# Kernel tuning notes

Measured on AMD Instinct MI355X. Metric: run time of the kernel, lower is better.

Reference implementation:

```python
import jax, jax.numpy as jnp
import numpy as np

N_ITEM, N_USER = 100000, 50000
D, H = 128, 8
DH = D // H
E1, E2 = 500000, 250000
NCNT = 51  # num_cnt_embeddings = cnt.max()+1
EPS = 1e-5


def setup_inputs() -> dict:
    key = jax.random.key(0)
    ks = jax.random.split(key, 32)
    r = lambda i, s: jax.random.normal(ks[i], s, dtype=jnp.float32)
    w = lambda i, s: jax.random.normal(ks[i], s, dtype=jnp.float32) * (1.0 / np.sqrt(s[-1]))
    return {
        # node features
        "ft_item": r(0, (N_ITEM, D)),
        "ft_user": r(1, (N_USER, D)),
        # hetero-level batch norm params (training-mode batch stats)
        "bn_g_item": jnp.ones((D,), jnp.float32), "bn_b_item": jnp.zeros((D,), jnp.float32),
        "bn_g_user": jnp.ones((D,), jnp.float32), "bn_b_user": jnp.zeros((D,), jnp.float32),
        # etype 'i2i' (item -> item), has cnt edge embedding
        "Wq1": w(2, (D, D)), "bq1": jnp.zeros((D,), jnp.float32),
        "Wk1": w(3, (D, D)), "Wv1": w(4, (D, D)),
        "ae1": r(5, (1, D)),
        "emb_cnt1": r(6, (NCNT, D)) * 0.1,
        # etype 'u2i' (user -> item), no cnt
        "Wq2": w(7, (D, D)), "bq2": jnp.zeros((D,), jnp.float32),
        "Wk2": w(8, (D, D)), "Wv2": w(9, (D, D)),
        "ae2": r(10, (1, D)),
        # vtype 'item' output transforms
        "W_agg": w(11, (D, D)), "b_agg": jnp.zeros((D,), jnp.float32),
        "W_self": w(12, (D, D)),
        # edges (eid order)
        "uid1": jax.random.randint(ks[13], (E1,), 0, N_ITEM, dtype=jnp.int32),
        "vid1": jax.random.randint(ks[14], (E1,), 0, N_ITEM, dtype=jnp.int32),
        "cnt1": jax.random.randint(ks[15], (E1,), 0, NCNT, dtype=jnp.int32),
        "uid2": jax.random.randint(ks[16], (E2,), 0, N_USER, dtype=jnp.int32),
        "vid2": jax.random.randint(ks[17], (E2,), 0, N_ITEM, dtype=jnp.int32),
    }


def _bn(x, g, b):
    mu = x.mean(0)
    var = x.var(0)
    return (x - mu) * jax.lax.rsqrt(var + EPS) * g + b


def _edge_scores(q_src, k_dst, uid, vid, attn_e, ft_e=None):
    # u_add_v gather, optional edge feature, gated per-head score [E, H]
    e = q_src[uid] + k_dst[vid]
    if ft_e is not None:
        e = e + ft_e
    e = attn_e * jax.nn.sigmoid(e)
    return e.reshape(-1, H, DH).sum(-1)


def reference(ft_item, ft_user, bn_g_item, bn_b_item, bn_g_user, bn_b_user,
              Wq1, bq1, Wk1, Wv1, ae1, emb_cnt1,
              Wq2, bq2, Wk2, Wv2, ae2,
              W_agg, b_agg, W_self,
              uid1, vid1, cnt1, uid2, vid2):
    xi = _bn(ft_item, bn_g_item, bn_b_item)   # item features (src and dst)
    xu = _bn(ft_user, bn_g_user, bn_b_user)   # user features (src only)

    # etype 'i2i': utype=item, vtype=item (ft_dst = xi, full graph)
    q1 = xi @ Wq1.T + bq1
    k1 = xi @ Wk1.T
    v1 = (xi @ Wv1.T).reshape(N_ITEM, H, DH)
    e1 = _edge_scores(q1, k1, uid1, vid1, ae1, ft_e=emb_cnt1[cnt1])  # [E1, H]

    # etype 'u2i': utype=user, vtype=item
    q2 = xu @ Wq2.T + bq2
    k2 = xi @ Wk2.T
    v2 = (xu @ Wv2.T).reshape(N_USER, H, DH)
    e2 = _edge_scores(q2, k2, uid2, vid2, ae2)  # [E2, H]

    # combined heterograph: offset user src ids by num item src nodes
    src = jnp.concatenate([uid1, uid2 + N_ITEM])
    dst = jnp.concatenate([vid1, vid2])
    val = jnp.concatenate([v1, v2], axis=0)        # [N_ITEM+N_USER, H, DH]
    sc = jnp.concatenate([e1, e2], axis=0)         # [E, H]

    # edge_softmax over incoming edges of each dst node (per head)
    m = jax.lax.stop_gradient(jax.ops.segment_max(sc, dst, num_segments=N_ITEM))
    ex = jnp.exp(sc - m[dst])
    s = jax.ops.segment_sum(ex, dst, num_segments=N_ITEM)
    a = ex / s[dst]                                # [E, H]

    # u_mul_e_sum: weighted scatter-sum of source values to dst
    agg = jax.ops.segment_sum(val[src] * a[:, :, None], dst,
                              num_segments=N_ITEM).reshape(N_ITEM, D)

    return jax.nn.relu(agg @ W_agg.T + b_agg + xi @ W_self.T)
```

## Files before the change

kernel.cpp:

```cpp
#include <hip/hip_runtime.h>
#include <hip/hip_bf16.h>

#define N_ITEM 100000
#define N_USER 50000
#define N_ALL  150000
#define E1N 500000
#define E2N 250000
#define EALL (E1N + E2N)
#define NPAD 100352

static constexpr size_t OFF_STATS = 0;
static constexpr size_t OFF_HIST  = 2048;
static constexpr size_t OFF_SCALE = OFF_HIST + (size_t)NPAD * 4;
static constexpr size_t OFF_M     = OFF_SCALE + 2048;
static constexpr size_t OFF_EMBB  = OFF_M + 64;
static constexpr size_t OFF_WPACK = OFF_EMBB + 13312;
static constexpr size_t OFF_QC    = OFF_WPACK + 8ull * 32768ull;
static constexpr size_t OFF_VC    = OFF_QC + (size_t)N_ALL * 256;
static constexpr size_t OFF_K1    = OFF_VC + (size_t)N_ALL * 256;
static constexpr size_t OFF_K2    = OFF_K1 + (size_t)N_ITEM * 256;
static constexpr size_t OFF_SELF  = OFF_K2 + (size_t)N_ITEM * 256;
static constexpr size_t OFF_START = OFF_SELF + (size_t)N_ITEM * 256;
static constexpr size_t OFF_CURSOR= OFF_START + (size_t)NPAD * 4;
static constexpr size_t OFF_BSUM  = OFF_CURSOR + (size_t)NPAD * 4;
static constexpr size_t OFF_ORD   = OFF_BSUM + 1024;
static constexpr size_t OFF_AGG   = OFF_ORD + (size_t)EALL * 8 + 128;

__device__ __forceinline__ float bf2f(unsigned short u) {
    return __uint_as_float(((unsigned)u) << 16);
}
__device__ __forceinline__ unsigned short f2bf(float f) {
    unsigned u = __float_as_uint(f);
    u += 0x7fffu + ((u >> 16) & 1u);
    return (unsigned short)(u >> 16);
}

typedef __attribute__((ext_vector_type(8))) short bf16x8;
typedef __attribute__((ext_vector_type(4))) float f32x4;

struct ProArgs {
    const float* w[8];
    const float* ft_item;
    const float* ft_user;
    const float* emb;
    const int* vid1;
    const int* vid2;
};
#define PRO_STAT 384
#define PRO_HIST 733
#define PRO_PACK 64
#define PRO_EMB  7

__global__ __launch_bounds__(256) void prologue(ProArgs A, char* __restrict__ ws) {
    __shared__ float r1[4][128], r2[4][128];
    int b = blockIdx.x, tid = threadIdx.x;
    if (b < PRO_STAT) {
        int type = (b >= 256) ? 1 : 0;
        int xb = type ? (b - 256) : b;
        int nb = type ? 128 : 256;
        const float* x = type ? A.ft_user : A.ft_item;
        int N = type ? N_USER : N_ITEM;
        float* sum = (float*)(ws + OFF_STATS) + type * 256;
        float* sq  = sum + 128;
        int c4 = (tid & 31) * 4;
        int rg = tid >> 5;
        int step = nb * 8;
        float s0 = 0.f, s1 = 0.f, s2 = 0.f, s3 = 0.f;
        float q0 = 0.f, q1 = 0.f, q2 = 0.f, q3 = 0.f;
        #pragma unroll 4
        for (int r = xb * 8 + rg; r < N; r += step) {
            float4 v = *(const float4*)(x + (size_t)r * 128 + c4);
            s0 += v.x; s1 += v.y; s2 += v.z; s3 += v.w;
            q0 = fmaf(v.x, v.x, q0); q1 = fmaf(v.y, v.y, q1);
            q2 = fmaf(v.z, v.z, q2); q3 = fmaf(v.w, v.w, q3);
        }
        s0 += __shfl_xor(s0, 32); s1 += __shfl_xor(s1, 32);
        s2 += __shfl_xor(s2, 32); s3 += __shfl_xor(s3, 32);
        q0 += __shfl_xor(q0, 32); q1 += __shfl_xor(q1, 32);
        q2 += __shfl_xor(q2, 32); q3 += __shfl_xor(q3, 32);
        int wv = tid >> 6;
        if ((tid & 63) < 32) {
            *(float4*)&r1[wv][c4] = make_float4(s0, s1, s2, s3);
            *(float4*)&r2[wv][c4] = make_float4(q0, q1, q2, q3);
        }
        __syncthreads();
        if (tid < 128) {
            float a  = r1[0][tid] + r1[1][tid] + r1[2][tid] + r1[3][tid];
            float bb = r2[0][tid] + r2[1][tid] + r2[2][tid] + r2[3][tid];
            atomicAdd(&sum[tid], a);
            atomicAdd(&sq[tid], bb);
        }
    } else if (b < PRO_STAT + PRO_HIST) {
        int e4 = ((b - PRO_STAT) * 256 + tid) * 4;
        if (e4 < EALL) {
            int* hist = (int*)(ws + OFF_HIST);
            int4 v;
            if (e4 < E1N) v = *(const int4*)(A.vid1 + e4);
            else          v = *(const int4*)(A.vid2 + (e4 - E1N));
            atomicAdd(&hist[v.x], 1);
            atomicAdd(&hist[v.y], 1);
            atomicAdd(&hist[v.z], 1);
            atomicAdd(&hist[v.w], 1);
        }
    } else if (b < PRO_STAT + PRO_HIST + PRO_PACK) {
        unsigned short* dst = (unsigned short*)(ws + OFF_WPACK);
        int gid = (b - PRO_STAT - PRO_HIST) * 256 + tid;
        int m = gid >> 11, rem = gid & 2047;
        int t = rem >> 8, kt = (rem >> 6) & 3, lane = rem & 63;
        int n = t * 16 + (lane & 15);
        int k0 = kt * 32 + (lane >> 4) * 8;
        const float* wrow = A.w[m] + n * 128 + k0;
        float4 w0 = *(const float4*)wrow;
        float4 w1 = *(const float4*)(wrow + 4);
        ushort4 o0 = make_ushort4(f2bf(w0.x), f2bf(w0.y), f2bf(w0.z), f2bf(w0.w));
        ushort4 o1 = make_ushort4(f2bf(w1.x), f2bf(w1.y), f2bf(w1.z), f2bf(w1.w));
        *(ushort4*)(dst + (size_t)gid * 8)     = o0;
        *(ushort4*)(dst + (size_t)gid * 8 + 4) = o1;
    } else {
        int gid = (b - PRO_STAT - PRO_HIST - PRO_PACK) * 256 + tid;
        if (gid * 4 < 51 * 128) {
            float4 v = *(const float4*)(A.emb + gid * 4);
            ushort4 o = make_ushort4(f2bf(v.x), f2bf(v.y), f2bf(v.z), f2bf(v.w));
            *(ushort4*)((unsigned short*)(ws + OFF_EMBB) + gid * 4) = o;
        }
    }
}

__global__ __launch_bounds__(1024) void scan_partial(char* __restrict__ ws) {
    __shared__ int sd[1024];
    const int* hist = (const int*)(ws + OFF_HIST);
    int* start  = (int*)(ws + OFF_START);
    int* cursor = (int*)(ws + OFF_CURSOR);
    int* bsum   = (int*)(ws + OFF_BSUM);
    int t = threadIdx.x;
    int gid = blockIdx.x * 1024 + t;
    int v = hist[gid];
    sd[t] = v;
    __syncthreads();
    #pragma unroll
    for (int off = 1; off < 1024; off <<= 1) {
        int x = (t >= off) ? sd[t - off] : 0;
        __syncthreads();
        sd[t] += x;
        __syncthreads();
    }
    int ex = sd[t] - v;
    start[gid] = ex;
    cursor[gid] = ex;
    if (t == 1023) bsum[blockIdx.x] = sd[t];
}

__global__ __launch_bounds__(256) void mid(const float* __restrict__ g_i, const float* __restrict__ b_i,
                                           const float* __restrict__ g_u, const float* __restrict__ b_u,
                                           const float* __restrict__ ae1, const float* __restrict__ ae2,
                                           char* __restrict__ ws) {
    __shared__ int sd[128];
    int t = threadIdx.x;
    if (blockIdx.x == 0) {
        const float* stats = (const float*)(ws + OFF_STATS);
        float* scale = (float*)(ws + OFF_SCALE);
        float* M     = (float*)(ws + OFF_M);
        int type = t >> 7, c = t & 127;
        float N = type ? (float)N_USER : (float)N_ITEM;
        float su = stats[type * 256 + c];
        float sq = stats[type * 256 + 128 + c];
        float mu = su / N;
        float var = sq / N - mu * mu;
        float rstd = rsqrtf(var + 1e-5f);
        float g = type ? g_u[c] : g_i[c];
        float b = type ? b_u[c] : b_i[c];
        scale[type * 256 + c]       = g * rstd;
        scale[type * 256 + 128 + c] = b - mu * g * rstd;
        if (t < 8) {
            float m1 = 0.f, m2 = 0.f;
            for (int j = 0; j < 16; j++) {
                m1 += fmaxf(ae1[t * 16 + j], 0.f);
                m2 += fmaxf(ae2[t * 16 + j], 0.f);
            }
            M[t] = fmaxf(m1, m2);
        }
    } else {
        int* bsum = (int*)(ws + OFF_BSUM);
        int v = 0;
        if (t < 128) { v = (t < 98) ? bsum[t] : 0; sd[t] = v; }
        __syncthreads();
        #pragma unroll
        for (int off = 1; off < 128; off <<= 1) {
            int x = 0;
            if (t < 128 && t >= off) x = sd[t - off];
            __syncthreads();
            if (t < 128) sd[t] += x;
            __syncthreads();
        }
        if (t < 98) bsum[t] = sd[t] - v;
    }
}

struct TArgs {
    const float* x;
    const float* bias0;
    int N;
    int scaleOff;
    int nmat;
    int wtIdx[5];
    unsigned short* out[5];
};
struct ScArgs {
    const int* uid1; const int* vid1; const int* cnt1;
    const int* uid2; const int* vid2;
};

#define TB_I 782
#define TB_U 391
#define SC_B 733

__global__ __launch_bounds__(256, 5) void transform(TArgs AI, TArgs AU, ScArgs S, char* __restrict__ ws) {
    int b = blockIdx.x;
    if (b >= TB_I + TB_U) {
        int e0 = ((b - TB_I - TB_U) * 256 + threadIdx.x) * 4;
        if (e0 < EALL) {
            int* cursor = (int*)(ws + OFF_CURSOR);
            const int* bsum = (const int*)(ws + OFF_BSUM);
            int2* ord = (int2*)(ws + OFF_ORD);
            int4 u, c, d;
            if (e0 < E1N) {
                u = *(const int4*)(S.uid1 + e0);
                d = *(const int4*)(S.vid1 + e0);
                c = *(const int4*)(S.cnt1 + e0);
            } else {
                int ee = e0 - E1N;
                u = *(const int4*)(S.uid2 + ee);
                d = *(const int4*)(S.vid2 + ee);
                u.x += N_ITEM; u.y += N_ITEM; u.z += N_ITEM; u.w += N_ITEM;
                c = make_int4(-1, -1, -1, -1);
            }
            int us[4] = {u.x, u.y, u.z, u.w};
            int ds[4] = {d.x, d.y, d.z, d.w};
            int cs[4] = {c.x, c.y, c.z, c.w};
            #pragma unroll
            for (int j = 0; j < 4; j++) {
                int dst = ds[j];
                int pos = atomicAdd(&cursor[dst], 1) + bsum[dst >> 10];
                int2 rec; rec.x = us[j]; rec.y = cs[j];
                ord[pos] = rec;
            }
        }
        return;
    }
    const TArgs& A = (b < TB_I) ? AI : AU;
    int blk = (b < TB_I) ? b : b - TB_I;

    const unsigned short* wpack = (const unsigned short*)(ws + OFF_WPACK);
    const float* scaleb = (const float*)(ws + OFF_SCALE) + A.scaleOff;
    int tid = threadIdx.x, lane = tid & 63;
    int wv = tid >> 6;
    int l16 = lane & 15, quad = lane >> 4;
    int base = blk * 128 + wv * 32;

    bf16x8 bfr[2][4];
    #pragma unroll
    for (int kt = 0; kt < 4; kt++) {
        int c0 = kt * 32 + quad * 8;
        float4 sc0 = *(const float4*)(scaleb + c0);
        float4 sc1 = *(const float4*)(scaleb + c0 + 4);
        float4 bi0 = *(const float4*)(scaleb + 128 + c0);
        float4 bi1 = *(const float4*)(scaleb + 128 + c0 + 4);
        #pragma unroll
        for (int it = 0; it < 2; it++) {
            int gr = base + it * 16 + l16;
            bf16x8 f = {0, 0, 0, 0, 0, 0, 0, 0};
            if (gr < A.N) {
                const float* p = A.x + (size_t)gr * 128 + c0;
                float4 v0 = *(const float4*)p;
                float4 v1 = *(const float4*)(p + 4);
                f[0] = (short)f2bf(fmaf(v0.x, sc0.x, bi0.x));
                f[1] = (short)f2bf(fmaf(v0.y, sc0.y, bi0.y));
                f[2] = (short)f2bf(fmaf(v0.z, sc0.z, bi0.z));
                f[3] = (short)f2bf(fmaf(v0.w, sc0.w, bi0.w));
                f[4] = (short)f2bf(fmaf(v1.x, sc1.x, bi1.x));
                f[5] = (short)f2bf(fmaf(v1.y, sc1.y, bi1.y));
                f[6] = (short)f2bf(fmaf(v1.z, sc1.z, bi1.z));
                f[7] = (short)f2bf(fmaf(v1.w, sc1.w, bi1.w));
            }
            bfr[it][kt] = f;
        }
    }

    int gr0 = base + l16;
    int gr1 = base + 16 + l16;
    bool in0 = gr0 < A.N, in1 = gr1 < A.N;

    for (int m = 0; m < A.nmat; m++) {
        const unsigned short* wp = wpack + (size_t)A.wtIdx[m] * 16384;
        unsigned short* outp = A.out[m];
        const float* bias = (m == 0) ? A.bias0 : nullptr;
        #pragma unroll
        for (int nt = 0; nt < 8; nt++) {
            bf16x8 a4[4];
            #pragma unroll
            for (int kt = 0; kt < 4; kt++)
                a4[kt] = *(const bf16x8*)(wp + (size_t)((nt * 4 + kt) * 64 + lane) * 8);
            f32x4 acc0 = {0.f, 0.f, 0.f, 0.f};
            if (bias) {
                float4 bv = *(const float4*)(bias + nt * 16 + quad * 4);
                acc0[0] = bv.x; acc0[1] = bv.y; acc0[2] = bv.z; acc0[3] = bv.w;
            }
            f32x4 acc1 = acc0;
            #pragma unroll
            for (int kt = 0; kt < 4; kt++) {
                acc0 = __builtin_amdgcn_mfma_f32_16x16x32_bf16(a4[kt], bfr[0][kt], acc0, 0, 0, 0);
                acc1 = __builtin_amdgcn_mfma_f32_16x16x32_bf16(a4[kt], bfr[1][kt], acc1, 0, 0, 0);
            }
            ushort4 o0 = make_ushort4(f2bf(acc0[0]), f2bf(acc0[1]), f2bf(acc0[2]), f2bf(acc0[3]));
            ushort4 o1 = make_ushort4(f2bf(acc1[0]), f2bf(acc1[1]), f2bf(acc1[2]), f2bf(acc1[3]));
            int co = nt * 16 + quad * 4;
            if (in0) *(ushort4*)(outp + (size_t)gr0 * 128 + co) = o0;
            if (in1) *(ushort4*)(outp + (size_t)gr1 * 128 + co) = o1;
        }
    }
}

__global__ __launch_bounds__(256, 8) void edge_agg(const float* __restrict__ ae1, const float* __restrict__ ae2,
                                                   char* __restrict__ ws) {
    const unsigned short* qc = (const unsigned short*)(ws + OFF_QC);
    const unsigned short* vc = (const unsigned short*)(ws + OFF_VC);
    const unsigned short* k1 = (const unsigned short*)(ws + OFF_K1);
    const unsigned short* k2 = (const unsigned short*)(ws + OFF_K2);
    const unsigned short* embb = (const unsigned short*)(ws + OFF_EMBB);
    const int* start = (const int*)(ws + OFF_START);
    const int* bsum  = (const int*)(ws + OFF_BSUM);
    const int2* ord = (const int2*)(ws + OFF_ORD);
    const float* M = (const float*)(ws + OFF_M);
    float* agg = (float*)(ws + OFF_AGG);

    int tid = threadIdx.x;
    int lane = tid & 63;
    int half = lane >> 5;
    int l = lane & 31;
    int d0 = l << 2;
    int h = l >> 2;
    int dst = blockIdx.x * 4 + (tid >> 6);
    if (dst >= N_ITEM) return;

    float mh = M[h];
    float4 ae1v = *(const float4*)(ae1 + d0);
    float4 ae2v = *(const float4*)(ae2 + d0);
    ushort4 k1p = *(const ushort4*)(k1 + (size_t)dst * 128 + d0);
    ushort4 k2p = *(const ushort4*)(k2 + (size_t)dst * 128 + d0);
    float4 k1v = make_float4(bf2f(k1p.x), bf2f(k1p.y), bf2f(k1p.z), bf2f(k1p.w));
    float4 k2v = make_float4(bf2f(k2p.x), bf2f(k2p.y), bf2f(k2p.z), bf2f(k2p.w));

    int beg = start[dst] + bsum[dst >> 10];
    int end = start[dst + 1] + bsum[(dst + 1) >> 10];
    float a0 = 0.f, a1 = 0.f, a2 = 0.f, a3 = 0.f, s = 0.f;

    int i = beg + half;
    if (i < end) {
        int2 rec = ord[i];
        while (true) {
            int inext = i + 2;
            int ipf = (inext < end) ? inext : (end - 1);
            int2 recn = ord[ipf];
            bool t1 = rec.y >= 0;
            ushort4 qp = *(const ushort4*)(qc + (size_t)rec.x * 128 + d0);
            ushort4 vp = *(const ushort4*)(vc + (size_t)rec.x * 128 + d0);
            ushort4 ep = *(const ushort4*)(embb + (size_t)(t1 ? rec.y : 0) * 128 + d0);
            float x0 = bf2f(qp.x) + (t1 ? k1v.x + bf2f(ep.x) : k2v.x);
            float x1 = bf2f(qp.y) + (t1 ? k1v.y + bf2f(ep.y) : k2v.y);
            float x2 = bf2f(qp.z) + (t1 ? k1v.z + bf2f(ep.z) : k2v.z);
            float x3 = bf2f(qp.w) + (t1 ? k1v.w + bf2f(ep.w) : k2v.w);
            float4 ae = t1 ? ae1v : ae2v;
            float t = ae.x * __builtin_amdgcn_rcpf(1.f + __expf(-x0))
                    + ae.y * __builtin_amdgcn_rcpf(1.f + __expf(-x1))
                    + ae.z * __builtin_amdgcn_rcpf(1.f + __expf(-x2))
                    + ae.w * __builtin_amdgcn_rcpf(1.f + __expf(-x3));
            t += __shfl_xor(t, 1);
            t += __shfl_xor(t, 2);
            float ex = __expf(t - mh);
            s += ex;
            a0 = fmaf(ex, bf2f(vp.x), a0);
            a1 = fmaf(ex, bf2f(vp.y), a1);
            a2 = fmaf(ex, bf2f(vp.z), a2);
            a3 = fmaf(ex, bf2f(vp.w), a3);
            if (inext >= end) break;
            i = inext; rec = recn;
        }
    }
    s  += __shfl_xor(s, 32);
    a0 += __shfl_xor(a0, 32);
    a1 += __shfl_xor(a1, 32);
    a2 += __shfl_xor(a2, 32);
    a3 += __shfl_xor(a3, 32);
    if (half == 0) {
        float inv = (s > 0.f) ? __builtin_amdgcn_rcpf(s) : 0.f;
        float4 o = make_float4(a0 * inv, a1 * inv, a2 * inv, a3 * inv);
        *(float4*)(agg + (size_t)dst * 128 + d0) = o;
    }
}

#define FPITCH 132

__global__ __launch_bounds__(256) void final_mfma(const float* __restrict__ b_agg,
                                                  float* __restrict__ out, char* __restrict__ ws) {
    __shared__ float stg[4][16 * FPITCH];
    const float* agg = (const float*)(ws + OFF_AGG);
    const unsigned short* selft = (const unsigned short*)(ws + OFF_SELF);
    const unsigned short* wp = (const unsigned short*)(ws + OFF_WPACK) + 7ull * 16384;
    int tid = threadIdx.x, lane = tid & 63, wv = tid >> 6;
    int l16 = lane & 15, quad = lane >> 4;
    int base = blockIdx.x * 256 + wv * 64;
    float* st = stg[wv];

    bf16x8 bfr[4][4];
    #pragma unroll
    for (int it = 0; it < 4; it++) {
        int gr = base + it * 16 + l16;
        #pragma unroll
        for (int kt = 0; kt < 4; kt++) {
            bf16x8 f = {0, 0, 0, 0, 0, 0, 0, 0};
            if (gr < N_ITEM) {
                const float* p = agg + (size_t)gr * 128 + kt * 32 + quad * 8;
                float4 v0 = *(const float4*)p;
                float4 v1 = *(const float4*)(p + 4);
                f[0] = (short)f2bf(v0.x); f[1] = (short)f2bf(v0.y);
                f[2] = (short)f2bf(v0.z); f[3] = (short)f2bf(v0.w);
                f[4] = (short)f2bf(v1.x); f[5] = (short)f2bf(v1.y);
                f[6] = (short)f2bf(v1.z); f[7] = (short)f2bf(v1.w);
            }
            bfr[it][kt] = f;
        }
    }

    #pragma unroll
    for (int it = 0; it < 4; it++) {
        #pragma unroll
        for (int nt = 0; nt < 8; nt++) {
            bf16x8 a4[4];
            #pragma unroll
            for (int kt = 0; kt < 4; kt++)
                a4[kt] = *(const bf16x8*)(wp + (size_t)((nt * 4 + kt) * 64 + lane) * 8);
            float4 bv = *(const float4*)(b_agg + nt * 16 + quad * 4);
            f32x4 acc = {bv.x, bv.y, bv.z, bv.w};
            #pragma unroll
            for (int kt = 0; kt < 4; kt++)
                acc = __builtin_amdgcn_mfma_f32_16x16x32_bf16(a4[kt], bfr[it][kt], acc, 0, 0, 0);
            *(f32x4*)(st + l16 * FPITCH + nt * 16 + quad * 4) = acc;
        }
        #pragma unroll
        for (int i = 0; i < 8; i++) {
            int chunk = i * 64 + lane;
            int row = chunk >> 5, c4 = (chunk & 31) * 4;
            int gr = base + it * 16 + row;
            if (gr < N_ITEM) {
                float4 v = *(const float4*)(st + row * FPITCH + c4);
                size_t idx = (size_t)gr * 128 + c4;
                ushort4 sf = *(const ushort4*)(selft + idx);
                float4 o;
                o.x = fmaxf(v.x + bf2f(sf.x), 0.f);
                o.y = fmaxf(v.y + bf2f(sf.y), 0.f);
                o.z = fmaxf(v.z + bf2f(sf.z), 0.f);
                o.w = fmaxf(v.w + bf2f(sf.w), 0.f);
                *(float4*)(out + idx) = o;
            }
        }
    }
}

extern "C" void kernel_launch(void* const* d_in, const int* in_sizes, int n_in,
                              void* d_out, int out_size, void* d_ws, size_t ws_size,
                              hipStream_t stream) {
    char* ws = (char*)d_ws;

    const float* ft_item = (const float*)d_in[0];
    const float* ft_user = (const float*)d_in[1];
    const float* bng_i = (const float*)d_in[2];
    const float* bnb_i = (const float*)d_in[3];
    const float* bng_u = (const float*)d_in[4];
    const float* bnb_u = (const float*)d_in[5];
    const float* Wq1 = (const float*)d_in[6];
    const float* bq1 = (const float*)d_in[7];
    const float* Wk1 = (const float*)d_in[8];
    const float* Wv1 = (const float*)d_in[9];
    const float* ae1 = (const float*)d_in[10];
    const float* emb = (const float*)d_in[11];
    const float* Wq2 = (const float*)d_in[12];
    const float* bq2 = (const float*)d_in[13];
    const float* Wk2 = (const float*)d_in[14];
    const float* Wv2 = (const float*)d_in[15];
    const float* ae2 = (const float*)d_in[16];
    const float* W_agg = (const float*)d_in[17];
    const float* b_agg = (const float*)d_in[18];
    const float* W_self = (const float*)d_in[19];
    const int* uid1 = (const int*)d_in[20];
    const int* vid1 = (const int*)d_in[21];
    const int* cnt1 = (const int*)d_in[22];
    const int* uid2 = (const int*)d_in[23];
    const int* vid2 = (const int*)d_in[24];
    float* out = (float*)d_out;

    hipMemsetAsync(ws + OFF_STATS, 0, 2048 + (size_t)NPAD * 4, stream);

    ProArgs pa;
    pa.w[0] = Wq1; pa.w[1] = Wk1; pa.w[2] = Wv1; pa.w[3] = Wk2;
    pa.w[4] = W_self; pa.w[5] = Wq2; pa.w[6] = Wv2; pa.w[7] = W_agg;
    pa.ft_item = ft_item; pa.ft_user = ft_user; pa.emb = emb;
    pa.vid1 = vid1; pa.vid2 = vid2;
    prologue<<<PRO_STAT + PRO_HIST + PRO_PACK + PRO_EMB, 256, 0, stream>>>(pa, ws);

    scan_partial<<<98, 1024, 0, stream>>>(ws);

    mid<<<2, 256, 0, stream>>>(bng_i, bnb_i, bng_u, bnb_u, ae1, ae2, ws);

    TArgs ti, tu;
    ti.x = ft_item; ti.bias0 = bq1; ti.N = N_ITEM; ti.scaleOff = 0; ti.nmat = 5;
    ti.wtIdx[0] = 0; ti.wtIdx[1] = 1; ti.wtIdx[2] = 2; ti.wtIdx[3] = 3; ti.wtIdx[4] = 4;
    unsigned short* QC = (unsigned short*)(ws + OFF_QC);
    unsigned short* VC = (unsigned short*)(ws + OFF_VC);
    ti.out[0] = QC;
    ti.out[1] = (unsigned short*)(ws + OFF_K1);
    ti.out[2] = VC;
    ti.out[3] = (unsigned short*)(ws + OFF_K2);
    ti.out[4] = (unsigned short*)(ws + OFF_SELF);
    tu.x = ft_user; tu.bias0 = bq2; tu.N = N_USER; tu.scaleOff = 256; tu.nmat = 2;
    tu.wtIdx[0] = 5; tu.wtIdx[1] = 6; tu.wtIdx[2] = 0; tu.wtIdx[3] = 0; tu.wtIdx[4] = 0;
    tu.out[0] = QC + (size_t)N_ITEM * 128;
    tu.out[1] = VC + (size_t)N_ITEM * 128;
    tu.out[2] = tu.out[3] = tu.out[4] = tu.out[0];
    ScArgs sa;
    sa.uid1 = uid1; sa.vid1 = vid1; sa.cnt1 = cnt1; sa.uid2 = uid2; sa.vid2 = vid2;
    transform<<<TB_I + TB_U + SC_B, 256, 0, stream>>>(ti, tu, sa, ws);

    edge_agg<<<(N_ITEM + 3) / 4, 256, 0, stream>>>(ae1, ae2, ws);

    final_mfma<<<(N_ITEM + 255) / 256, 256, 0, stream>>>(b_agg, out, ws);
}
```

Measured before the change: 432.5 us.

## Process four edges per wave with 8-wide bf16 loads and store agg as bf16

The edge aggregation kernel now splits each wave into four 16-lane slots, each handling one edge with 8 features per lane via 16-byte bf16 loads, instead of two 32-lane halves with 4 features per lane. The aggregated output is written as bf16, so the final MFMA kernel reads it directly without a float-to-bf16 conversion, halving that intermediate's traffic. This gives more edges in flight per wave and fewer, wider gather loads, at the cost of more registers (launch bound occupancy hint lowered from 8 to 6) and an extra cross-slot reduction.

```diff
diff --git a/kernel.cpp b/kernel.cpp
--- a/kernel.cpp
+++ b/kernel.cpp
@@ -320,7 +320,7 @@
     }
 }
 
-__global__ __launch_bounds__(256, 8) void edge_agg(const float* __restrict__ ae1, const float* __restrict__ ae2,
+__global__ __launch_bounds__(256, 6) void edge_agg(const float* __restrict__ ae1, const float* __restrict__ ae2,
                                                    char* __restrict__ ws) {
     const unsigned short* qc = (const unsigned short*)(ws + OFF_QC);
     const unsigned short* vc = (const unsigned short*)(ws + OFF_VC);
@@ -331,70 +331,85 @@
     const int* bsum  = (const int*)(ws + OFF_BSUM);
     const int2* ord = (const int2*)(ws + OFF_ORD);
     const float* M = (const float*)(ws + OFF_M);
-    float* agg = (float*)(ws + OFF_AGG);
+    unsigned short* aggb = (unsigned short*)(ws + OFF_AGG);
 
     int tid = threadIdx.x;
     int lane = tid & 63;
-    int half = lane >> 5;
-    int l = lane & 31;
-    int d0 = l << 2;
-    int h = l >> 2;
+    int slot = lane >> 4;
+    int l = lane & 15;
+    int d0 = l << 3;
+    int h = l >> 1;
     int dst = blockIdx.x * 4 + (tid >> 6);
     if (dst >= N_ITEM) return;
 
     float mh = M[h];
-    float4 ae1v = *(const float4*)(ae1 + d0);
-    float4 ae2v = *(const float4*)(ae2 + d0);
-    ushort4 k1p = *(const ushort4*)(k1 + (size_t)dst * 128 + d0);
-    ushort4 k2p = *(const ushort4*)(k2 + (size_t)dst * 128 + d0);
-    float4 k1v = make_float4(bf2f(k1p.x), bf2f(k1p.y), bf2f(k1p.z), bf2f(k1p.w));
-    float4 k2v = make_float4(bf2f(k2p.x), bf2f(k2p.y), bf2f(k2p.z), bf2f(k2p.w));
+    float ae1v[8], ae2v[8], k1v[8], k2v[8];
+    {
+        float4 t0 = *(const float4*)(ae1 + d0);
+        float4 t1 = *(const float4*)(ae1 + d0 + 4);
+        ae1v[0]=t0.x; ae1v[1]=t0.y; ae1v[2]=t0.z; ae1v[3]=t0.w;
+        ae1v[4]=t1.x; ae1v[5]=t1.y; ae1v[6]=t1.z; ae1v[7]=t1.w;
+        float4 t2 = *(const float4*)(ae2 + d0);
+        float4 t3 = *(const float4*)(ae2 + d0 + 4);
+        ae2v[0]=t2.x; ae2v[1]=t2.y; ae2v[2]=t2.z; ae2v[3]=t2.w;
+        ae2v[4]=t3.x; ae2v[5]=t3.y; ae2v[6]=t3.z; ae2v[7]=t3.w;
+        bf16x8 k1p = *(const bf16x8*)(k1 + (size_t)dst * 128 + d0);
+        bf16x8 k2p = *(const bf16x8*)(k2 + (size_t)dst * 128 + d0);
+        #pragma unroll
+        for (int j = 0; j < 8; j++) {
+            k1v[j] = bf2f((unsigned short)k1p[j]);
+            k2v[j] = bf2f((unsigned short)k2p[j]);
+        }
+    }
 
     int beg = start[dst] + bsum[dst >> 10];
     int end = start[dst + 1] + bsum[(dst + 1) >> 10];
-    float a0 = 0.f, a1 = 0.f, a2 = 0.f, a3 = 0.f, s = 0.f;
-
-    int i = beg + half;
+    float a[8] = {0.f, 0.f, 0.f, 0.f, 0.f, 0.f, 0.f, 0.f};
+    float s = 0.f;
+
+    int i = beg + slot;
     if (i < end) {
         int2 rec = ord[i];
         while (true) {
-            int inext = i + 2;
+            int inext = i + 4;
             int ipf = (inext < end) ? inext : (end - 1);
             int2 recn = ord[ipf];
-            bool t1 = rec.y >= 0;
-            ushort4 qp = *(const ushort4*)(qc + (size_t)rec.x * 128 + d0);
-            ushort4 vp = *(const ushort4*)(vc + (size_t)rec.x * 128 + d0);
-            ushort4 ep = *(const ushort4*)(embb + (size_t)(t1 ? rec.y : 0) * 128 + d0);
-            float x0 = bf2f(qp.x) + (t1 ? k1v.x + bf2f(ep.x) : k2v.x);
-            float x1 = bf2f(qp.y) + (t1 ? k1v.y + bf2f(ep.y) : k2v.y);
-            float x2 = bf2f(qp.z) + (t1 ? k1v.z + bf2f(ep.z) : k2v.z);
-            float x3 = bf2f(qp.w) + (t1 ? k1v.w + bf2f(ep.w) : k2v.w);
-            float4 ae = t1 ? ae1v : ae2v;
-            float t = ae.x * __builtin_amdgcn_rcpf(1.f + __expf(-x0))
-                    + ae.y * __builtin_amdgcn_rcpf(1.f + __expf(-x1))
-                    + ae.z * __builtin_amdgcn_rcpf(1.f + __expf(-x2))
-                    + ae.w * __builtin_amdgcn_rcpf(1.f + __expf(-x3));
+            bool t1e = rec.y >= 0;
+            bf16x8 qp = *(const bf16x8*)(qc + (size_t)rec.x * 128 + d0);
+            bf16x8 vp = *(const bf16x8*)(vc + (size_t)rec.x * 128 + d0);
+            bf16x8 ep = *(const bf16x8*)(embb + (size_t)(t1e ? rec.y : 0) * 128 + d0);
+            float t = 0.f;
+            #pragma unroll
+            for (int j = 0; j < 8; j++) {
+                float kv = t1e ? (k1v[j] + bf2f((unsigned short)ep[j])) : k2v[j];
+                float x = bf2f((unsigned short)qp[j]) + kv;
+                float sg = __builtin_amdgcn_rcpf(1.f + __expf(-x));
+                t = fmaf(t1e ? ae1v[j] : ae2v[j], sg, t);
+            }
             t += __shfl_xor(t, 1);
-            t += __shfl_xor(t, 2);
             float ex = __expf(t - mh);
             s += ex;
-            a0 = fmaf(ex, bf2f(vp.x), a0);
-            a1 = fmaf(ex, bf2f(vp.y), a1);
-            a2 = fmaf(ex, bf2f(vp.z), a2);
-            a3 = fmaf(ex, bf2f(vp.w), a3);
+            #pragma unroll
+            for (int j = 0; j < 8; j++)
+                a[j] = fmaf(ex, bf2f((unsigned short)vp[j]), a[j]);
             if (inext >= end) break;
             i = inext; rec = recn;
         }
     }
-    s  += __shfl_xor(s, 32);
-    a0 += __shfl_xor(a0, 32);
-    a1 += __shfl_xor(a1, 32);
-    a2 += __shfl_xor(a2, 32);
-    a3 += __shfl_xor(a3, 32);
-    if (half == 0) {
+    s += __shfl_xor(s, 16);
+    s += __shfl_xor(s, 32);
+    #pragma unroll
+    for (int j = 0; j < 8; j++) {
+        a[j] += __shfl_xor(a[j], 16);
+        a[j] += __shfl_xor(a[j], 32);
+    }
+    if (slot == 0) {
         float inv = (s > 0.f) ? __builtin_amdgcn_rcpf(s) : 0.f;
-        float4 o = make_float4(a0 * inv, a1 * inv, a2 * inv, a3 * inv);
-        *(float4*)(agg + (size_t)dst * 128 + d0) = o;
+        bf16x8 o;
+        #pragma unroll
+        for (int j = 0; j < 8; j++)
+            o[j] = (short)f2bf(a[j] * inv);
+        *(bf16x8*)(aggb + (size_t)dst * 128 + d0) = o;
     }
 }
 
@@ -403,7 +418,7 @@
 __global__ __launch_bounds__(256) void final_mfma(const float* __restrict__ b_agg,
                                                   float* __restrict__ out, char* __restrict__ ws) {
     __shared__ float stg[4][16 * FPITCH];
-    const float* agg = (const float*)(ws + OFF_AGG);
+    const unsigned short* aggb = (const unsigned short*)(ws + OFF_AGG);
     const unsigned short* selft = (const unsigned short*)(ws + OFF_SELF);
     const unsigned short* wp = (const unsigned short*)(ws + OFF_WPACK) + 7ull * 16384;
     int tid = threadIdx.x, lane = tid & 63, wv = tid >> 6;
@@ -418,15 +433,8 @@
         #pragma unroll
         for (int kt = 0; kt < 4; kt++) {
             bf16x8 f = {0, 0, 0, 0, 0, 0, 0, 0};
-            if (gr < N_ITEM) {
-                const float* p = agg + (size_t)gr * 128 + kt * 32 + quad * 8;
-                float4 v0 = *(const float4*)p;
-                float4 v1 = *(const float4*)(p + 4);
-                f[0] = (short)f2bf(v0.x); f[1] = (short)f2bf(v0.y);
-                f[2] = (short)f2bf(v0.z); f[3] = (short)f2bf(v0.w);
-                f[4] = (short)f2bf(v1.x); f[5] = (short)f2bf(v1.y);
-                f[6] = (short)f2bf(v1.z); f[7] = (short)f2bf(v1.w);
-            }
+            if (gr < N_ITEM)
+                f = *(const bf16x8*)(aggb + (size_t)gr * 128 + kt * 32 + quad * 8);
             bfr[it][kt] = f;
         }
     }
```

After: 432.4 us. Within noise of the previous version (-0.0%).
